# Performance work log

Measured on AMD Instinct MI355X. Metric: run time of the kernel, lower is better.

## Reference

```python
import jax, jax.numpy as jnp
import numpy as np

S, B, E, H = 2048, 4, 512, 8
HD = E // H


def setup_inputs() -> dict:
    key = jax.random.key(0)
    ks = jax.random.split(key, 5)
    scale = 1.0 / np.sqrt(E)
    return {
        "query": jax.random.normal(ks[0], (S, B, E), jnp.float32),
        "key": jax.random.normal(ks[1], (S, B, E), jnp.float32),
        "value": jax.random.normal(ks[2], (S, B, E), jnp.float32),
        "in_proj_weight": jax.random.normal(ks[3], (3 * E, E), jnp.float32) * scale,
        "in_proj_bias": jnp.zeros((3 * E,), jnp.float32),
        "out_proj_weight": jax.random.normal(ks[4], (E, E), jnp.float32) * scale,
        "out_proj_bias": jnp.zeros((E,), jnp.float32),
    }


def reference(query, key, value, in_proj_weight, in_proj_bias, out_proj_weight, out_proj_bias):
    tgt_len, bsz, embed_dim = query.shape
    src_len = key.shape[0]
    # Quirk of this module: first chunk (w_qk) projects BOTH q and k; third chunk projects v.
    w_qk = in_proj_weight[:embed_dim]
    w_v = in_proj_weight[2 * embed_dim:]
    b_qk = in_proj_bias[:embed_dim]
    b_v = in_proj_bias[2 * embed_dim:]
    q = query @ w_qk.T + b_qk          # [S, B, E]
    k = key @ w_qk.T + b_qk
    v = value @ w_v.T + b_v
    # (S, B, E) -> (B*H, S, HD)
    def split_heads(x, n):
        return x.reshape(n, bsz * H, HD).transpose(1, 0, 2)
    q = split_heads(q, tgt_len) / jnp.sqrt(jnp.asarray(HD, q.dtype))
    k = split_heads(k, src_len)
    v = split_heads(v, src_len)
    scores = jnp.einsum("bqd,bkd->bqk", q, k)          # [B*H, S, S] full score matrix
    attn = jax.nn.softmax(scores, axis=-1)
    out = jnp.einsum("bqk,bkd->bqd", attn, v)          # [B*H, S, HD]
    out = out.transpose(1, 0, 2).reshape(tgt_len * bsz, embed_dim)
    out = out @ out_proj_weight.T + out_proj_bias
    return out.reshape(tgt_len, bsz, embed_dim)
```

## Files before the change

kernel.cpp:

```cpp
#include <hip/hip_runtime.h>
#include <hip/hip_bf16.h>

typedef __attribute__((ext_vector_type(8))) short s16x8;
typedef __attribute__((ext_vector_type(4))) short s16x4;
typedef __attribute__((ext_vector_type(4))) float f32x4;
typedef __attribute__((ext_vector_type(4))) _Float16 f16x4;

#if __has_builtin(__builtin_amdgcn_mfma_f32_16x16x16bf16_1k)
#define PV_USE_BF16 1
#else
#define PV_USE_BF16 0
#endif

#define S_LEN 2048
#define EMB   512
#define MROWS 8192

__device__ __forceinline__ float bf2f(short x) {
    union { float f; unsigned u; } z; z.u = ((unsigned)(unsigned short)x) << 16; return z.f;
}
__device__ __forceinline__ short f2bf(float f) {
    union { float f; unsigned u; } z; z.f = f;
    unsigned r = z.u + 0x7FFF + ((z.u >> 16) & 1);
    return (short)(r >> 16);
}
__device__ __forceinline__ short f2bf_fast(float f) {
    union { float f; unsigned u; } z; z.f = f;
    return (short)((z.u + 0x8000u) >> 16);
}
__device__ __forceinline__ short f2v(float f) {
#if PV_USE_BF16
    return f2bf(f);
#else
    union { _Float16 h; short s; } u; u.h = (_Float16)f; return u.s;
#endif
}

template<int AF32, int BF32>
__device__ __forceinline__ void gemm_mainloop(const void* __restrict__ Ag,
                                              const void* __restrict__ Bg,
                                              short* sA, short* sB,
                                              f32x4 acc[4][4], int K)
{
    const int tid  = threadIdx.x;
    const int lane = tid & 63;
    const int wv   = tid >> 6;
    const int l15  = lane & 15, quad = lane >> 4;
    const int wm   = (wv >> 1) * 64, wn = (wv & 1) * 64;

    f32x4 afr[4], bfr[4];
    s16x8 ahr[2], bhr[2];

    auto loadT = [&](const void* G, int kt, f32x4* fr, s16x8* hr, int F32) {
        if (F32) {
#pragma unroll
            for (int p = 0; p < 4; ++p) {
                int c = tid + p * 256;
                fr[p] = *(const f32x4*)((const float*)G + (size_t)(c >> 3) * K + kt + (c & 7) * 4);
            }
        } else {
#pragma unroll
            for (int p = 0; p < 2; ++p) {
                int c = tid + p * 256;
                hr[p] = *(const s16x8*)((const short*)G + (size_t)(c >> 2) * K + kt + (c & 3) * 8);
            }
        }
    };
    auto commitT = [&](short* s, f32x4* fr, s16x8* hr, int F32) {
        if (F32) {
#pragma unroll
            for (int p = 0; p < 4; ++p) {
                int c = tid + p * 256;
                s16x4 o4;
                o4[0] = f2bf_fast(fr[p][0]); o4[1] = f2bf_fast(fr[p][1]);
                o4[2] = f2bf_fast(fr[p][2]); o4[3] = f2bf_fast(fr[p][3]);
                *(s16x4*)(s + c * 4) = o4;
            }
        } else {
#pragma unroll
            for (int p = 0; p < 2; ++p) {
                int c = tid + p * 256;
                *(s16x8*)(s + c * 8) = hr[p];
            }
        }
    };

    loadT(Ag, 0, afr, ahr, AF32);
    loadT(Bg, 0, bfr, bhr, BF32);
    commitT(sA, afr, ahr, AF32);
    commitT(sB, bfr, bhr, BF32);
    __syncthreads();

    for (int kt = 0; kt < K; kt += 32) {
        const int ktn = (kt + 32 < K) ? kt + 32 : 0;
        loadT(Ag, ktn, afr, ahr, AF32);
        loadT(Bg, ktn, bfr, bhr, BF32);

        s16x8 aF[4], bF[4];
#pragma unroll
        for (int i = 0; i < 4; ++i)
            aF[i] = *(const s16x8*)(sA + (wm + i * 16 + l15) * 32 + quad * 8);
#pragma unroll
        for (int j = 0; j < 4; ++j)
            bF[j] = *(const s16x8*)(sB + (wn + j * 16 + l15) * 32 + quad * 8);
#pragma unroll
        for (int i = 0; i < 4; ++i)
#pragma unroll
            for (int j = 0; j < 4; ++j)
                acc[i][j] = __builtin_amdgcn_mfma_f32_16x16x32_bf16(aF[i], bF[j], acc[i][j], 0, 0, 0);

        __syncthreads();
        commitT(sA, afr, ahr, AF32);
        commitT(sB, bfr, bhr, BF32);
        __syncthreads();
    }
}

__global__ __launch_bounds__(256, 3) void qkv_proj(const float* __restrict__ query,
                                                   const float* __restrict__ key,
                                                   const float* __restrict__ value,
                                                   const float* __restrict__ W,
                                                   const float* __restrict__ bias,
                                                   short* __restrict__ q,
                                                   short* __restrict__ k,
                                                   short* __restrict__ v)
{
    __shared__ __align__(16) short sA[4096], sB[4096];
    const int z = blockIdx.z;
    const float* X  = (z == 0) ? query : (z == 1) ? key : value;
    const float* Wz = W    + (z == 2 ? (size_t)1024 * EMB : 0);
    const float* bz = bias + (z == 2 ? 1024 : 0);
    short* dst = (z == 0) ? q : (z == 1) ? k : v;
    const float scale = (z == 0) ? 0.125f : 1.0f;

    const int blockM = blockIdx.y * 128, blockN = blockIdx.x * 128;

    f32x4 acc[4][4];
#pragma unroll
    for (int i = 0; i < 4; ++i)
#pragma unroll
        for (int j = 0; j < 4; ++j)
            acc[i][j] = (f32x4){0.f, 0.f, 0.f, 0.f};

    gemm_mainloop<1, 1>(X + (size_t)blockM * EMB, Wz + (size_t)blockN * EMB,
                        sA, sB, acc, EMB);

    const int tid = threadIdx.x, lane = tid & 63, wv = tid >> 6;
    const int l15 = lane & 15, quad = lane >> 4;
    const int wm = (wv >> 1) * 64, wn = (wv & 1) * 64;

#pragma unroll
    for (int j = 0; j < 4; ++j) {
        int col = blockN + wn + j * 16 + l15;
        float bval = bz[col];
        int h = col >> 6, hd = col & 63;
#pragma unroll
        for (int i = 0; i < 4; ++i) {
#pragma unroll
            for (int r = 0; r < 4; ++r) {
                int row = blockM + wm + i * 16 + quad * 4 + r;
                int s = row >> 2, b = row & 3;
                float val = (acc[i][j][r] + bval) * scale;
                short bits = (z == 2) ? f2v(val) : f2bf(val);
                dst[((size_t)((b * 8 + h) * 2048 + s)) * 64 + hd] = bits;
            }
        }
    }
}

__global__ __launch_bounds__(256) void transpose_v(const short* __restrict__ v,
                                                   short* __restrict__ vt)
{
    __shared__ __align__(16) short t[64 * 68];
    const int bh = blockIdx.y, s0 = blockIdx.x * 64, tid = threadIdx.x;

#pragma unroll
    for (int p = 0; p < 2; ++p) {
        int r  = (tid >> 3) + p * 32;
        int cc = (tid & 7) * 8;
        s16x8 d = *(const s16x8*)(v + ((size_t)(bh * 2048 + s0 + r)) * 64 + cc);
        s16x4 lo = {d[0], d[1], d[2], d[3]};
        s16x4 hi = {d[4], d[5], d[6], d[7]};
        *(s16x4*)(t + r * 68 + cc)     = lo;
        *(s16x4*)(t + r * 68 + cc + 4) = hi;
    }
    __syncthreads();
#pragma unroll
    for (int p = 0; p < 2; ++p) {
        int hd = (tid >> 3) + p * 32;
        int so = (tid & 7) * 8;
        s16x8 d;
#pragma unroll
        for (int j = 0; j < 8; ++j) d[j] = t[(so + j) * 68 + hd];
        *(s16x8*)(vt + ((size_t)(bh * 64 + hd)) * 2048 + s0 + so) = d;
    }
}

__global__ __launch_bounds__(256, 4) void flash_attn(const short* __restrict__ q,
                                                     const short* __restrict__ k,
                                                     const short* __restrict__ vt,
                                                     short* __restrict__ attn)
{
    __shared__ __align__(16) short sK[64 * 72];
    __shared__ __align__(16) short sV[64 * 72];
    const int bh = blockIdx.x;
    const int q0 = blockIdx.y * 64;
    const int tid = threadIdx.x, wv = tid >> 6, lane = tid & 63;
    const int l15 = lane & 15, quad = lane >> 4;

    const short* qp = q + ((size_t)(bh * 2048 + q0 + wv * 16 + l15)) * 64 + quad * 8;
    s16x8 qf0 = *(const s16x8*)qp;
    s16x8 qf1 = *(const s16x8*)(qp + 32);

    const short* kg = k  + (size_t)bh * 2048 * 64;
    const short* vg = vt + (size_t)bh * 64 * 2048;

    const int r0 = tid >> 3,          c0 = (tid & 7) * 8;
    const int r1 = (tid + 256) >> 3,  c1 = ((tid + 256) & 7) * 8;

#if PV_USE_BF16
    typedef s16x4 pvec;
#else
    typedef f16x4 pvec;
#endif

    f32x4 o[4];
    float lsum = 0.f;
#pragma unroll
    for (int i = 0; i < 4; ++i) o[i] = (f32x4){0.f, 0.f, 0.f, 0.f};

    s16x8 ka = *(const s16x8*)(kg + (size_t)r0 * 64 + c0);
    s16x8 kb = *(const s16x8*)(kg + (size_t)r1 * 64 + c1);
    s16x8 va = *(const s16x8*)(vg + (size_t)r0 * 2048 + c0);
    s16x8 vb = *(const s16x8*)(vg + (size_t)r1 * 2048 + c1);
    *(s16x8*)(sK + r0 * 72 + c0) = ka;
    *(s16x8*)(sK + r1 * 72 + c1) = kb;
    *(s16x8*)(sV + r0 * 72 + c0) = va;
    *(s16x8*)(sV + r1 * 72 + c1) = vb;
    __syncthreads();

    for (int kt = 0; kt < 2048; kt += 64) {
        const int ktn = (kt + 64) & 2047;
        ka = *(const s16x8*)(kg + (size_t)(ktn + r0) * 64 + c0);
        kb = *(const s16x8*)(kg + (size_t)(ktn + r1) * 64 + c1);
        va = *(const s16x8*)(vg + (size_t)r0 * 2048 + ktn + c0);
        vb = *(const s16x8*)(vg + (size_t)r1 * 2048 + ktn + c1);

        f32x4 sc[4];
#pragma unroll
        for (int ct = 0; ct < 4; ++ct) {
            s16x8 kf0 = *(const s16x8*)(sK + (ct * 16 + l15) * 72 + quad * 8);
            s16x8 kf1 = *(const s16x8*)(sK + (ct * 16 + l15) * 72 + quad * 8 + 32);
            f32x4 c = (f32x4){0.f, 0.f, 0.f, 0.f};
            c = __builtin_amdgcn_mfma_f32_16x16x32_bf16(kf0, qf0, c, 0, 0, 0);
            c = __builtin_amdgcn_mfma_f32_16x16x32_bf16(kf1, qf1, c, 0, 0, 0);
            sc[ct] = c;
        }
        pvec pf[4];
#pragma unroll
        for (int ct = 0; ct < 4; ++ct)
#pragma unroll
            for (int r = 0; r < 4; ++r) {
                float p = __expf(sc[ct][r]);
                lsum += p;
#if PV_USE_BF16
                pf[ct][r] = f2bf_fast(p);
#else
                pf[ct][r] = (_Float16)p;
#endif
            }
#pragma unroll
        for (int nt = 0; nt < 4; ++nt)
#pragma unroll
            for (int ct = 0; ct < 4; ++ct) {
                pvec vf = *(const pvec*)(sV + (nt * 16 + l15) * 72 + ct * 16 + quad * 4);
#if PV_USE_BF16
                o[nt] = __builtin_amdgcn_mfma_f32_16x16x16bf16_1k(pf[ct], vf, o[nt], 0, 0, 0);
#else
                o[nt] = __builtin_amdgcn_mfma_f32_16x16x16f16(pf[ct], vf, o[nt], 0, 0, 0);
#endif
            }
        __syncthreads();
        *(s16x8*)(sK + r0 * 72 + c0) = ka;
        *(s16x8*)(sK + r1 * 72 + c1) = kb;
        *(s16x8*)(sV + r0 * 72 + c0) = va;
        *(s16x8*)(sV + r1 * 72 + c1) = vb;
        __syncthreads();
    }

    float s = lsum;
    s += __shfl_xor(s, 16, 64);
    s += __shfl_xor(s, 32, 64);
    float sinv = 1.0f / s;
    float inv[4];
#pragma unroll
    for (int r = 0; r < 4; ++r)
        inv[r] = __shfl(sinv, quad * 20 + r, 64);

    const int b = bh >> 3, h = bh & 7;
#pragma unroll
    for (int r = 0; r < 4; ++r) {
        int srow = q0 + wv * 16 + quad * 4 + r;
#pragma unroll
        for (int nt = 0; nt < 4; ++nt)
            attn[(size_t)(srow * 4 + b) * 512 + h * 64 + nt * 16 + l15] = f2bf(o[nt][r] * inv[r]);
    }
}

__global__ __launch_bounds__(256, 3) void out_proj(const short* __restrict__ attn,
                                                   const float* __restrict__ W,
                                                   const float* __restrict__ bias,
                                                   float* __restrict__ out)
{
    __shared__ __align__(16) short sA[4096], sB[4096];
    const int blockM = blockIdx.y * 128, blockN = blockIdx.x * 128;

    f32x4 acc[4][4];
#pragma unroll
    for (int i = 0; i < 4; ++i)
#pragma unroll
        for (int j = 0; j < 4; ++j)
            acc[i][j] = (f32x4){0.f, 0.f, 0.f, 0.f};

    gemm_mainloop<0, 1>(attn + (size_t)blockM * EMB, W + (size_t)blockN * EMB,
                        sA, sB, acc, EMB);

    const int tid = threadIdx.x, lane = tid & 63, wv = tid >> 6;
    const int l15 = lane & 15, quad = lane >> 4;
    const int wm = (wv >> 1) * 64, wn = (wv & 1) * 64;

#pragma unroll
    for (int j = 0; j < 4; ++j) {
        int col = blockN + wn + j * 16 + l15;
        float bval = bias[col];
#pragma unroll
        for (int i = 0; i < 4; ++i) {
#pragma unroll
            for (int r = 0; r < 4; ++r) {
                int row = blockM + wm + i * 16 + quad * 4 + r;
                out[(size_t)row * 512 + col] = acc[i][j][r] + bval;
            }
        }
    }
}

extern "C" void kernel_launch(void* const* d_in, const int* in_sizes, int n_in,
                              void* d_out, int out_size, void* d_ws, size_t ws_size,
                              hipStream_t stream)
{
    const float* query = (const float*)d_in[0];
    const float* key   = (const float*)d_in[1];
    const float* value = (const float*)d_in[2];
    const float* ipw   = (const float*)d_in[3];
    const float* ipb   = (const float*)d_in[4];
    const float* opw   = (const float*)d_in[5];
    const float* opb   = (const float*)d_in[6];
    float* out = (float*)d_out;

    const size_t NELEM = (size_t)MROWS * EMB;
    short* q    = (short*)d_ws;
    short* k    = q + NELEM;
    short* vbuf = k + NELEM;
    short* vt   = (short*)d_out;

    qkv_proj   <<<dim3(4, 64, 3), 256, 0, stream>>>(query, key, value, ipw, ipb, q, k, vbuf);
    transpose_v<<<dim3(32, 32),   256, 0, stream>>>(vbuf, vt);
    flash_attn <<<dim3(32, 32),   256, 0, stream>>>(q, k, vt, vbuf);
    out_proj   <<<dim3(4, 64),    256, 0, stream>>>(vbuf, opw, opb, out);
}
```

Baseline: 213.1 us.

## Fuse V transpose into QKV projection, widen GEMM blocks, use exp2

```diff
diff --git a/kernel.cpp b/kernel.cpp
--- a/kernel.cpp
+++ b/kernel.cpp
@@ -12,6 +12,12 @@
 #define PV_USE_BF16 0
 #endif
 
+#if __has_builtin(__builtin_amdgcn_exp2f)
+#define EXP2F(x) __builtin_amdgcn_exp2f(x)
+#else
+#define EXP2F(x) exp2f(x)
+#endif
+
 #define S_LEN 2048
 #define EMB   512
 #define MROWS 8192
@@ -40,48 +46,40 @@
 __device__ __forceinline__ void gemm_mainloop(const void* __restrict__ Ag,
                                               const void* __restrict__ Bg,
                                               short* sA, short* sB,
-                                              f32x4 acc[4][4], int K)
+                                              f32x4 acc[2][4], int K)
 {
     const int tid  = threadIdx.x;
     const int lane = tid & 63;
     const int wv   = tid >> 6;
     const int l15  = lane & 15, quad = lane >> 4;
-    const int wm   = (wv >> 1) * 64, wn = (wv & 1) * 64;
-
-    f32x4 afr[4], bfr[4];
-    s16x8 ahr[2], bhr[2];
-
-    auto loadT = [&](const void* G, int kt, f32x4* fr, s16x8* hr, int F32) {
+    const int wm   = (wv >> 1) * 32, wn = (wv & 1) * 64;
+
+    f32x4 afr[2], bfr[2];
+    s16x8 ahr, bhr;
+
+    auto loadT = [&](const void* G, int kt, f32x4* fr, s16x8& hr, int F32) {
         if (F32) {
 #pragma unroll
-            for (int p = 0; p < 4; ++p) {
-                int c = tid + p * 256;
+            for (int p = 0; p < 2; ++p) {
+                int c = tid + p * 512;
                 fr[p] = *(const f32x4*)((const float*)G + (size_t)(c >> 3) * K + kt + (c & 7) * 4);
             }
         } else {
+            hr = *(const s16x8*)((const short*)G + (size_t)(tid >> 2) * K + kt + (tid & 3) * 8);
+        }
+    };
+    auto commitT = [&](short* s, f32x4* fr, s16x8& hr, int F32) {
+        if (F32) {
 #pragma unroll
             for (int p = 0; p < 2; ++p) {
-                int c = tid + p * 256;
-                hr[p] = *(const s16x8*)((const short*)G + (size_t)(c >> 2) * K + kt + (c & 3) * 8);
-            }
-        }
-    };
-    auto commitT = [&](short* s, f32x4* fr, s16x8* hr, int F32) {
-        if (F32) {
-#pragma unroll
-            for (int p = 0; p < 4; ++p) {
-                int c = tid + p * 256;
+                int c = tid + p * 512;
                 s16x4 o4;
                 o4[0] = f2bf_fast(fr[p][0]); o4[1] = f2bf_fast(fr[p][1]);
                 o4[2] = f2bf_fast(fr[p][2]); o4[3] = f2bf_fast(fr[p][3]);
                 *(s16x4*)(s + c * 4) = o4;
             }
         } else {
-#pragma unroll
-            for (int p = 0; p < 2; ++p) {
-                int c = tid + p * 256;
-                *(s16x8*)(s + c * 8) = hr[p];
-            }
+            *(s16x8*)(s + tid * 8) = hr;
         }
     };
 
@@ -96,15 +94,15 @@
         loadT(Ag, ktn, afr, ahr, AF32);
         loadT(Bg, ktn, bfr, bhr, BF32);
 
-        s16x8 aF[4], bF[4];
-#pragma unroll
-        for (int i = 0; i < 4; ++i)
+        s16x8 aF[2], bF[4];
+#pragma unroll
+        for (int i = 0; i < 2; ++i)
             aF[i] = *(const s16x8*)(sA + (wm + i * 16 + l15) * 32 + quad * 8);
 #pragma unroll
         for (int j = 0; j < 4; ++j)
             bF[j] = *(const s16x8*)(sB + (wn + j * 16 + l15) * 32 + quad * 8);
 #pragma unroll
-        for (int i = 0; i < 4; ++i)
+        for (int i = 0; i < 2; ++i)
 #pragma unroll
             for (int j = 0; j < 4; ++j)
                 acc[i][j] = __builtin_amdgcn_mfma_f32_16x16x32_bf16(aF[i], bF[j], acc[i][j], 0, 0, 0);
@@ -116,28 +114,27 @@
     }
 }
 
-__global__ __launch_bounds__(256, 3) void qkv_proj(const float* __restrict__ query,
+__global__ __launch_bounds__(512, 4) void qkv_proj(const float* __restrict__ query,
                                                    const float* __restrict__ key,
                                                    const float* __restrict__ value,
                                                    const float* __restrict__ W,
                                                    const float* __restrict__ bias,
                                                    short* __restrict__ q,
                                                    short* __restrict__ k,
-                                                   short* __restrict__ v)
+                                                   short* __restrict__ vt)
 {
     __shared__ __align__(16) short sA[4096], sB[4096];
     const int z = blockIdx.z;
     const float* X  = (z == 0) ? query : (z == 1) ? key : value;
     const float* Wz = W    + (z == 2 ? (size_t)1024 * EMB : 0);
     const float* bz = bias + (z == 2 ? 1024 : 0);
-    short* dst = (z == 0) ? q : (z == 1) ? k : v;
-    const float scale = (z == 0) ? 0.125f : 1.0f;
-
-    const int blockM = blockIdx.y * 128, blockN = blockIdx.x * 128;
-
-    f32x4 acc[4][4];
-#pragma unroll
-    for (int i = 0; i < 4; ++i)
+    const float scale = (z == 0) ? 0.125f * 1.44269504f : 1.0f;
+
+    const int blockM = blockIdx.x * 128, blockN = blockIdx.y * 128;
+
+    f32x4 acc[2][4];
+#pragma unroll
+    for (int i = 0; i < 2; ++i)
 #pragma unroll
         for (int j = 0; j < 4; ++j)
             acc[i][j] = (f32x4){0.f, 0.f, 0.f, 0.f};
@@ -147,7 +144,7 @@
 
     const int tid = threadIdx.x, lane = tid & 63, wv = tid >> 6;
     const int l15 = lane & 15, quad = lane >> 4;
-    const int wm = (wv >> 1) * 64, wn = (wv & 1) * 64;
+    const int wm = (wv >> 1) * 32, wn = (wv & 1) * 64;
 
 #pragma unroll
     for (int j = 0; j < 4; ++j) {
@@ -155,44 +152,21 @@
         float bval = bz[col];
         int h = col >> 6, hd = col & 63;
 #pragma unroll
-        for (int i = 0; i < 4; ++i) {
+        for (int i = 0; i < 2; ++i) {
 #pragma unroll
             for (int r = 0; r < 4; ++r) {
                 int row = blockM + wm + i * 16 + quad * 4 + r;
                 int s = row >> 2, b = row & 3;
                 float val = (acc[i][j][r] + bval) * scale;
-                short bits = (z == 2) ? f2v(val) : f2bf(val);
-                dst[((size_t)((b * 8 + h) * 2048 + s)) * 64 + hd] = bits;
-            }
-        }
-    }
-}
-
-__global__ __launch_bounds__(256) void transpose_v(const short* __restrict__ v,
-                                                   short* __restrict__ vt)
-{
-    __shared__ __align__(16) short t[64 * 68];
-    const int bh = blockIdx.y, s0 = blockIdx.x * 64, tid = threadIdx.x;
-
-#pragma unroll
-    for (int p = 0; p < 2; ++p) {
-        int r  = (tid >> 3) + p * 32;
-        int cc = (tid & 7) * 8;
-        s16x8 d = *(const s16x8*)(v + ((size_t)(bh * 2048 + s0 + r)) * 64 + cc);
-        s16x4 lo = {d[0], d[1], d[2], d[3]};
-        s16x4 hi = {d[4], d[5], d[6], d[7]};
-        *(s16x4*)(t + r * 68 + cc)     = lo;
-        *(s16x4*)(t + r * 68 + cc + 4) = hi;
-    }
-    __syncthreads();
-#pragma unroll
-    for (int p = 0; p < 2; ++p) {
-        int hd = (tid >> 3) + p * 32;
-        int so = (tid & 7) * 8;
-        s16x8 d;
-#pragma unroll
-        for (int j = 0; j < 8; ++j) d[j] = t[(so + j) * 68 + hd];
-        *(s16x8*)(vt + ((size_t)(bh * 64 + hd)) * 2048 + s0 + so) = d;
+                int bh = b * 8 + h;
+                if (z == 2) {
+                    vt[((size_t)(bh * 64 + hd)) * 2048 + s] = f2v(val);
+                } else {
+                    short* dst = (z == 0) ? q : k;
+                    dst[((size_t)(bh * 2048 + s)) * 64 + hd] = f2bf(val);
+                }
+            }
+        }
     }
 }
 
@@ -261,7 +235,7 @@
         for (int ct = 0; ct < 4; ++ct)
 #pragma unroll
             for (int r = 0; r < 4; ++r) {
-                float p = __expf(sc[ct][r]);
+                float p = EXP2F(sc[ct][r]);
                 lsum += p;
 #if PV_USE_BF16
                 pf[ct][r] = f2bf_fast(p);
@@ -307,17 +281,17 @@
     }
 }
 
-__global__ __launch_bounds__(256, 3) void out_proj(const short* __restrict__ attn,
+__global__ __launch_bounds__(512, 4) void out_proj(const short* __restrict__ attn,
                                                    const float* __restrict__ W,
                                                    const float* __restrict__ bias,
                                                    float* __restrict__ out)
 {
     __shared__ __align__(16) short sA[4096], sB[4096];
-    const int blockM = blockIdx.y * 128, blockN = blockIdx.x * 128;
-
-    f32x4 acc[4][4];
-#pragma unroll
-    for (int i = 0; i < 4; ++i)
+    const int blockM = blockIdx.x * 128, blockN = blockIdx.y * 128;
+
+    f32x4 acc[2][4];
+#pragma unroll
+    for (int i = 0; i < 2; ++i)
 #pragma unroll
         for (int j = 0; j < 4; ++j)
             acc[i][j] = (f32x4){0.f, 0.f, 0.f, 0.f};
@@ -327,14 +301,14 @@
 
     const int tid = threadIdx.x, lane = tid & 63, wv = tid >> 6;
     const int l15 = lane & 15, quad = lane >> 4;
-    const int wm = (wv >> 1) * 64, wn = (wv & 1) * 64;
+    const int wm = (wv >> 1) * 32, wn = (wv & 1) * 64;
 
 #pragma unroll
     for (int j = 0; j < 4; ++j) {
         int col = blockN + wn + j * 16 + l15;
         float bval = bias[col];
 #pragma unroll
-        for (int i = 0; i < 4; ++i) {
+        for (int i = 0; i < 2; ++i) {
 #pragma unroll
             for (int r = 0; r < 4; ++r) {
                 int row = blockM + wm + i * 16 + quad * 4 + r;
@@ -360,11 +334,10 @@
     const size_t NELEM = (size_t)MROWS * EMB;
     short* q    = (short*)d_ws;
     short* k    = q + NELEM;
-    short* vbuf = k + NELEM;
+    short* attn = k + NELEM;
     short* vt   = (short*)d_out;
 
-    qkv_proj   <<<dim3(4, 64, 3), 256, 0, stream>>>(query, key, value, ipw, ipb, q, k, vbuf);
-    transpose_v<<<dim3(32, 32),   256, 0, stream>>>(vbuf, vt);
-    flash_attn <<<dim3(32, 32),   256, 0, stream>>>(q, k, vt, vbuf);
-    out_proj   <<<dim3(4, 64),    256, 0, stream>>>(vbuf, opw, opb, out);
-}
+    qkv_proj  <<<dim3(64, 4, 3), 512, 0, stream>>>(query, key, value, ipw, ipb, q, k, vt);
+    flash_attn<<<dim3(32, 32),   256, 0, stream>>>(q, k, vt, attn);
+    out_proj  <<<dim3(64, 4),    512, 0, stream>>>(attn, opw, opb, out);
+}
```

New measurement: 212.1 us. No clear change (-0.5%).
